# Kernel optimization log

Measured on AMD Instinct MI355X. Metric: run time of the kernel, lower is better.

## Reference

```python
import jax, jax.numpy as jnp
import numpy as np

B, S, D = 8, 2048, 512
MINF = 20000.0  # matches tf code's -20000.0 mask constant


def setup_inputs() -> dict:
    key = jax.random.key(0)
    k1, k2, k3 = jax.random.split(key, 3)
    x1 = jax.random.normal(k1, (B, S, D), dtype=jnp.float32)
    x2 = jax.random.normal(k2, (B, S, D), dtype=jnp.float32)
    # glorot_normal init for the learned (S, S) positional kernel
    std = np.sqrt(2.0 / (S + S)).astype(np.float32)
    kernel = jax.random.normal(k3, (S, S), dtype=jnp.float32) * std
    return {"x1": x1, "x2": x2, "kernel": kernel}


def reference(x1, x2, kernel):
    S_ = kernel.shape[0]
    # tf.matmul(kernel, inputs[i]) broadcasts (S,S) @ (B,S,D) -> (B,S,D)
    h1 = jnp.einsum('st,btd->bsd', kernel, x1)
    h2 = jnp.einsum('st,btd->bsd', kernel, x2)
    # att_scores: (B, S, S)
    scores = jnp.einsum('bsd,btd->bst', h1, h2)
    d_k = jnp.asarray(S_, dtype=scores.dtype) ** 0.5
    # upper_m[i,j] = -20000 for j > i (strictly upper), else 0; added BEFORE scaling
    row = jnp.arange(S_)
    mask = jnp.where(row[None, :] > row[:, None], -MINF, 0.0).astype(scores.dtype)
    attn = jax.nn.softmax((scores + mask) / d_k, axis=-1)
    # note: output attends over h1 (not h2), as in the original code
    return jnp.einsum('bst,btd->bsd', attn, h1)
```

## Files before the change

kernel.cpp:

```cpp
#include <hip/hip_runtime.h>
#include <hip/hip_bf16.h>

#define S_DIM 2048
#define D_DIM 512
#define B_DIM 8
#define SCALE 0.02209708691207961f

typedef __hip_bfloat16 bf16;
typedef short bf16x8 __attribute__((ext_vector_type(8)));
typedef float f32x4 __attribute__((ext_vector_type(4)));

__device__ __forceinline__ unsigned short f2b(float f) {
  __hip_bfloat16 h = __float2bfloat16(f);
  return __builtin_bit_cast(unsigned short, h);
}
__device__ __forceinline__ float b2f(unsigned short s) {
  return __bfloat162float(__builtin_bit_cast(__hip_bfloat16, s));
}

__device__ __forceinline__ void load_lds16(const void* g, void* l) {
  __builtin_amdgcn_global_load_lds((const __attribute__((address_space(1))) void*)g,
                                   (__attribute__((address_space(3))) void*)l, 16, 0, 0);
}

__global__ void prep(const float* __restrict__ x1, const float* __restrict__ x2,
                     const float* __restrict__ km,
                     bf16* __restrict__ xt, bf16* __restrict__ Kbf,
                     float* __restrict__ rowsum) {
  const int z = blockIdx.z;
  const int tid = threadIdx.x;
  if (z == 16) {
    const int bid = blockIdx.y * 8 + blockIdx.x;
    const float4* p = (const float4*)km;
    bf16x8* o = (bf16x8*)Kbf;
#pragma unroll
    for (int it = 0; it < 8; it++) {
      int i = bid * 2048 + it * 256 + tid;
      float4 a = p[2 * i], b = p[2 * i + 1];
      bf16x8 r;
      r[0] = f2b(a.x); r[1] = f2b(a.y); r[2] = f2b(a.z); r[3] = f2b(a.w);
      r[4] = f2b(b.x); r[5] = f2b(b.y); r[6] = f2b(b.z); r[7] = f2b(b.w);
      o[i] = r;
    }
    if (bid < 8) {
      float4 zf = {0.0f, 0.0f, 0.0f, 0.0f};
      float4* rp = (float4*)(rowsum + bid * 2048);
      rp[tid * 2] = zf;
      rp[tid * 2 + 1] = zf;
    }
    return;
  }
  __shared__ unsigned short t[64][66];
  const float* in = (z < 8 ? x1 : x2) + (size_t)(z & 7) * (S_DIM * D_DIM);
  bf16* ob = xt + (size_t)z * (size_t)(D_DIM * S_DIM);
  const int r0 = blockIdx.y * 64;
  const int c0 = blockIdx.x * 64;
  const int lr = tid >> 4, lq = tid & 15;
#pragma unroll
  for (int i = 0; i < 4; i++) {
    int r = i * 16 + lr;
    float4 v = *(const float4*)(in + (size_t)(r0 + r) * D_DIM + c0 + lq * 4);
    t[lq * 4 + 0][r] = f2b(v.x);
    t[lq * 4 + 1][r] = f2b(v.y);
    t[lq * 4 + 2][r] = f2b(v.z);
    t[lq * 4 + 3][r] = f2b(v.w);
  }
  __syncthreads();
#pragma unroll
  for (int j = 0; j < 4; j++) {
    int d = j * 16 + lr;
    const unsigned short* p = &t[d][lq * 4];
    uint2 u;
    u.x = (unsigned)p[0] | ((unsigned)p[1] << 16);
    u.y = (unsigned)p[2] | ((unsigned)p[3] << 16);
    *(uint2*)(ob + (size_t)(c0 + d) * S_DIM + r0 + lq * 4) = u;
  }
}

__global__ __launch_bounds__(512, 2) void gemm_h(
    const bf16* __restrict__ A, const bf16* __restrict__ X, bf16* __restrict__ H) {
  extern __shared__ char smem[];
  const int pid = blockIdx.x;
  const int mt = pid & 7;
  const int r_ = pid >> 3;
  const int ntile = r_ & 1;
  const int item = r_ >> 1;
  const int m0 = mt * 256, n0 = ntile * 256;
  const bf16* Xi = X + (size_t)item * (D_DIM * S_DIM);
  bf16* Hi = H + (size_t)item * (S_DIM * D_DIM);

  const int tid = threadIdx.x;
  const int w = tid >> 6, L = tid & 63;
  const int l15 = L & 15, lhi = L >> 4;
  const int wr = w >> 2, wn = w & 3;

  const int srow = tid >> 2;
  const int sslot = ((tid & 3) ^ ((tid >> 3) & 3)) * 8;
  const bf16* pA[2];
  const bf16* pB[2];
#pragma unroll
  for (int ld = 0; ld < 2; ld++) {
    pA[ld] = A + (size_t)(m0 + ld * 128 + srow) * 2048 + sslot;
    pB[ld] = Xi + (size_t)(n0 + ld * 128 + srow) * 2048 + sslot;
  }

  char* A0 = smem;          char* A1 = smem + 16384;  char* A2 = smem + 32768;
  char* B0 = smem + 49152;  char* B1 = smem + 65536;  char* B2 = smem + 81920;

  auto stage = [&](int t2, char* dA, char* dB) {
#pragma unroll
    for (int ld = 0; ld < 2; ld++)
      load_lds16(pA[ld] + t2 * 32, dA + ld * 8192 + w * 1024);
#pragma unroll
    for (int ld = 0; ld < 2; ld++)
      load_lds16(pB[ld] + t2 * 32, dB + ld * 8192 + w * 1024);
  };

  const int xo = (lhi ^ ((l15 >> 1) & 3)) << 4;
  int offA[8], offB[4];
#pragma unroll
  for (int m = 0; m < 8; m++) offA[m] = (wr * 128 + m * 16 + l15) * 64 + xo;
#pragma unroll
  for (int n = 0; n < 4; n++) offB[n] = (wn * 64 + n * 16 + l15) * 64 + xo;

  f32x4 acc[8][4];
#pragma unroll
  for (int m = 0; m < 8; m++)
#pragma unroll
    for (int n = 0; n < 4; n++) acc[m][n] = (f32x4){0, 0, 0, 0};

  stage(0, A0, B0);
  stage(1, A1, B1);

#pragma unroll 1
  for (int t = 0; t < 64; ++t) {
    if (t < 63) asm volatile("s_waitcnt vmcnt(4)" ::: "memory");
    else        asm volatile("s_waitcnt vmcnt(0)" ::: "memory");
    __builtin_amdgcn_s_barrier();
    asm volatile("" ::: "memory");
    if (t < 62) stage(t + 2, A2, B2);

    bf16x8 af[8], bfv[4];
#pragma unroll
    for (int m = 0; m < 8; m++) af[m] = *(const bf16x8*)(A0 + offA[m]);
#pragma unroll
    for (int n = 0; n < 4; n++) bfv[n] = *(const bf16x8*)(B0 + offB[n]);
    __builtin_amdgcn_s_setprio(1);
#pragma unroll
    for (int m = 0; m < 8; m++)
#pragma unroll
      for (int n = 0; n < 4; n++)
        acc[m][n] = __builtin_amdgcn_mfma_f32_16x16x32_bf16(bfv[n], af[m], acc[m][n], 0, 0, 0);
    __builtin_amdgcn_s_setprio(0);

    char* tA = A0; A0 = A1; A1 = A2; A2 = tA;
    char* tB = B0; B0 = B1; B1 = B2; B2 = tB;
  }

#pragma unroll
  for (int m = 0; m < 8; m++) {
    int grow = m0 + wr * 128 + m * 16 + l15;
#pragma unroll
    for (int n = 0; n < 4; n++) {
      int gcol = n0 + wn * 64 + n * 16 + lhi * 4;
      uint2 u;
      u.x = ((unsigned)f2b(acc[m][n][1]) << 16) | f2b(acc[m][n][0]);
      u.y = ((unsigned)f2b(acc[m][n][3]) << 16) | f2b(acc[m][n][2]);
      *(uint2*)(Hi + (size_t)grow * D_DIM + gcol) = u;
    }
  }
}

__global__ __launch_bounds__(512, 2) void gemm_score(
    const bf16* __restrict__ H1, const bf16* __restrict__ H2,
    bf16* __restrict__ E, float* __restrict__ rowsum, bf16* __restrict__ H1T) {
  extern __shared__ char smem[];
  const int pid = blockIdx.x;
  const int tid = threadIdx.x;

  if (pid >= 288) {
    const int tb = pid - 288;
    const int half = tid >> 8;
    const int t5 = tid & 255;
    unsigned short (*tl)[66] = (unsigned short (*)[66])(smem + half * 8448);
    const int lr = t5 >> 4, lq = t5 & 15;
#pragma unroll 1
    for (int i = 0; i < 4; i++) {
      const int tile = tb * 8 + half * 4 + i;
      const int z = tile >> 8;
      const int rem = tile & 255;
      const int r0 = (rem >> 3) * 64;
      const int c0 = (rem & 7) * 64;
      const bf16* ib = H1 + (size_t)z * (S_DIM * D_DIM);
      bf16* ob = H1T + (size_t)z * (S_DIM * D_DIM);
#pragma unroll
      for (int j = 0; j < 4; j++) {
        int r = j * 16 + lr;
        uint2 v = *(const uint2*)(ib + (size_t)(r0 + r) * D_DIM + c0 + lq * 4);
        tl[lq * 4 + 0][r] = (unsigned short)(v.x & 0xffff);
        tl[lq * 4 + 1][r] = (unsigned short)(v.x >> 16);
        tl[lq * 4 + 2][r] = (unsigned short)(v.y & 0xffff);
        tl[lq * 4 + 3][r] = (unsigned short)(v.y >> 16);
      }
      __syncthreads();
#pragma unroll
      for (int j = 0; j < 4; j++) {
        int d = j * 16 + lr;
        const unsigned short* p = &tl[d][lq * 4];
        uint2 u;
        u.x = (unsigned)p[0] | ((unsigned)p[1] << 16);
        u.y = (unsigned)p[2] | ((unsigned)p[3] << 16);
        *(uint2*)(ob + (size_t)(c0 + d) * S_DIM + r0 + lq * 4) = u;
      }
      __syncthreads();
    }
    return;
  }

  const int b = pid & 7;
  const int tri = pid >> 3;
  int mt = (int)((sqrtf(8.0f * (float)tri + 1.0f) - 1.0f) * 0.5f);
  while ((mt + 1) * (mt + 2) / 2 <= tri) mt++;
  while (mt * (mt + 1) / 2 > tri) mt--;
  const int nt = tri - mt * (mt + 1) / 2;
  const int m0 = mt * 256, n0 = nt * 256;
  const bool diag = (mt == nt);
  const bf16* Ab = H1 + (size_t)b * S_DIM * D_DIM;
  const bf16* Bb = H2 + (size_t)b * S_DIM * D_DIM;
  bf16* Eb = E + (size_t)b * S_DIM * S_DIM;
  float* rs = rowsum + b * S_DIM;

  const int w = tid >> 6, L = tid & 63;
  const int l15 = L & 15, lhi = L >> 4;
  const int wr = w >> 2, wn = w & 3;

  const int srow = tid >> 2;
  const int sslot = ((tid & 3) ^ ((tid >> 3) & 3)) * 8;
  const bf16* pA[2];
  const bf16* pB[2];
#pragma unroll
  for (int ld = 0; ld < 2; ld++) {
    pA[ld] = Ab + (size_t)(m0 + ld * 128 + srow) * D_DIM + sslot;
    pB[ld] = Bb + (size_t)(n0 + ld * 128 + srow) * D_DIM + sslot;
  }

  auto stage = [&](int t) {
    char* dA = smem + (t & 1) * 16384;
    char* dB = smem + 32768 + (t & 1) * 16384;
#pragma unroll
    for (int ld = 0; ld < 2; ld++)
      load_lds16(pA[ld] + t * 32, dA + ld * 8192 + w * 1024);
#pragma unroll
    for (int ld = 0; ld < 2; ld++)
      load_lds16(pB[ld] + t * 32, dB + ld * 8192 + w * 1024);
  };

  const int xo = (lhi ^ ((l15 >> 1) & 3)) << 4;
  int offA[8], offB[4];
#pragma unroll
  for (int m = 0; m < 8; m++) offA[m] = (wr * 128 + m * 16 + l15) * 64 + xo;
#pragma unroll
  for (int n = 0; n < 4; n++) offB[n] = (wn * 64 + n * 16 + l15) * 64 + xo;

  f32x4 acc[8][4];
#pragma unroll
  for (int m = 0; m < 8; m++)
#pragma unroll
    for (int n = 0; n < 4; n++) acc[m][n] = (f32x4){0, 0, 0, 0};

  stage(0);
#pragma unroll 2
  for (int t = 0; t < 16; ++t) {
    __syncthreads();
    if (t + 1 < 16) stage(t + 1);
    const char* bA = smem + (t & 1) * 16384;
    const char* bB = smem + 32768 + (t & 1) * 16384;
    bf16x8 af[8], bfv[4];
#pragma unroll
    for (int m = 0; m < 8; m++) af[m] = *(const bf16x8*)(bA + offA[m]);
#pragma unroll
    for (int n = 0; n < 4; n++) bfv[n] = *(const bf16x8*)(bB + offB[n]);
    __builtin_amdgcn_s_setprio(1);
#pragma unroll
    for (int m = 0; m < 8; m++)
#pragma unroll
      for (int n = 0; n < 4; n++)
        acc[m][n] = __builtin_amdgcn_mfma_f32_16x16x32_bf16(bfv[n], af[m], acc[m][n], 0, 0, 0);
    __builtin_amdgcn_s_setprio(0);
  }

#pragma unroll
  for (int m = 0; m < 8; m++) {
    int sg = m0 + wr * 128 + m * 16 + l15;
    float rp = 0.0f;
#pragma unroll
    for (int n = 0; n < 4; n++) {
      int tg0 = n0 + wn * 64 + n * 16 + lhi * 4;
      unsigned short e[4];
#pragma unroll
      for (int r = 0; r < 4; r++) {
        float v = (!diag || (tg0 + r) <= sg) ? __expf(acc[m][n][r] * SCALE) : 0.0f;
        e[r] = f2b(v);
        rp += b2f(e[r]);
      }
      uint2 u;
      u.x = ((unsigned)e[1] << 16) | e[0];
      u.y = ((unsigned)e[3] << 16) | e[2];
      *(uint2*)(Eb + (size_t)sg * S_DIM + tg0) = u;
    }
    rp += __shfl_xor(rp, 16);
    rp += __shfl_xor(rp, 32);
    if (lhi == 0) atomicAdd(rs + sg, rp);
  }
}

__global__ __launch_bounds__(256, 2) void gemm_pv(
    const bf16* __restrict__ E, const bf16* __restrict__ H1T,
    const float* __restrict__ rowsum, float* __restrict__ out) {
  extern __shared__ char smem[];
  const int pid = blockIdx.x;
  const int b = pid & 7;
  const int r_ = pid >> 3;
  const int nt = r_ & 3;
  const int mb = r_ >> 2;
  const int mt = (mb < 8) ? 2 * mb : 31 - 2 * mb;
  const int m0 = mt * 128, n0 = nt * 128;
  const int NT = (mt + 1) * 4;
  const bf16* Ab = E + (size_t)b * S_DIM * S_DIM + (size_t)m0 * S_DIM;
  const bf16* Bb = H1T + (size_t)b * D_DIM * S_DIM + (size_t)n0 * S_DIM;
  const float* rs = rowsum + b * S_DIM;
  float* Cb = out + (size_t)b * S_DIM * D_DIM;

  const int tid = threadIdx.x;
  const int w = tid >> 6, L = tid & 63;
  const int l15 = L & 15, lhi = L >> 4;
  const int wr = w >> 1, wc = w & 1;

  const int srow = tid >> 2;
  const int sslot = ((tid & 3) ^ ((tid >> 3) & 3)) * 8;
  const bf16* pA[2];
  const bf16* pB[2];
#pragma unroll
  for (int ld = 0; ld < 2; ld++) {
    pA[ld] = Ab + (size_t)(ld * 64 + srow) * S_DIM + sslot;
    pB[ld] = Bb + (size_t)(ld * 64 + srow) * S_DIM + sslot;
  }

  char* A0 = smem;          char* A1 = smem + 8192;   char* A2 = smem + 16384;
  char* B0 = smem + 24576;  char* B1 = smem + 32768;  char* B2 = smem + 40960;

  auto stage = [&](int t2, char* dA, char* dB) {
#pragma unroll
    for (int ld = 0; ld < 2; ld++)
      load_lds16(pA[ld] + t2 * 32, dA + ld * 4096 + w * 1024);
#pragma unroll
    for (int ld = 0; ld < 2; ld++)
      load_lds16(pB[ld] + t2 * 32, dB + ld * 4096 + w * 1024);
  };

  const int xo = (lhi ^ ((l15 >> 1) & 3)) << 4;
  int offA[4], offB[4];
#pragma unroll
  for (int m = 0; m < 4; m++) offA[m] = (wr * 64 + m * 16 + l15) * 64 + xo;
#pragma unroll
  for (int n = 0; n < 4; n++) offB[n] = (wc * 64 + n * 16 + l15) * 64 + xo;

  f32x4 acc[4][4];
#pragma unroll
  for (int m = 0; m < 4; m++)
#pragma unroll
    for (int n = 0; n < 4; n++) acc[m][n] = (f32x4){0, 0, 0, 0};

  stage(0, A0, B0);
  stage(1, A1, B1);

#pragma unroll 1
  for (int t = 0; t < NT; ++t) {
    if (t < NT - 1) asm volatile("s_waitcnt vmcnt(4)" ::: "memory");
    else            asm volatile("s_waitcnt vmcnt(0)" ::: "memory");
    __builtin_amdgcn_s_barrier();
    asm volatile("" ::: "memory");
    if (t + 2 < NT) stage(t + 2, A2, B2);

    bf16x8 af[4], bfv[4];
#pragma unroll
    for (int m = 0; m < 4; m++) af[m] = *(const bf16x8*)(A0 + offA[m]);
#pragma unroll
    for (int n = 0; n < 4; n++) bfv[n] = *(const bf16x8*)(B0 + offB[n]);
    __builtin_amdgcn_s_setprio(1);
#pragma unroll
    for (int m = 0; m < 4; m++)
#pragma unroll
      for (int n = 0; n < 4; n++)
        acc[m][n] = __builtin_amdgcn_mfma_f32_16x16x32_bf16(bfv[n], af[m], acc[m][n], 0, 0, 0);
    __builtin_amdgcn_s_setprio(0);

    char* tA = A0; A0 = A1; A1 = A2; A2 = tA;
    char* tB = B0; B0 = B1; B1 = B2; B2 = tB;
  }

#pragma unroll
  for (int m = 0; m < 4; m++) {
    int sg = m0 + wr * 64 + m * 16 + l15;
    float inv = 1.0f / rs[sg];
#pragma unroll
    for (int n = 0; n < 4; n++) {
      int gcol = n0 + wc * 64 + n * 16 + lhi * 4;
      float4 o;
      o.x = acc[m][n][0] * inv;
      o.y = acc[m][n][1] * inv;
      o.z = acc[m][n][2] * inv;
      o.w = acc[m][n][3] * inv;
      *(float4*)(Cb + (size_t)sg * D_DIM + gcol) = o;
    }
  }
}

extern "C" void kernel_launch(void* const* d_in, const int* in_sizes, int n_in,
                              void* d_out, int out_size, void* d_ws, size_t ws_size,
                              hipStream_t stream) {
  const float* x1 = (const float*)d_in[0];
  const float* x2 = (const float*)d_in[1];
  const float* km = (const float*)d_in[2];
  float* out = (float*)d_out;
  char* ws = (char*)d_ws;
  bf16* E    = (bf16*)(ws);
  bf16* Kbf  = (bf16*)(ws);
  bf16* x1t  = (bf16*)(ws + (8ull << 20));
  bf16* h1n  = (bf16*)(ws + (64ull << 20));
  bf16* h2n  = (bf16*)(ws + (80ull << 20));
  bf16* h1t  = (bf16*)(ws + (96ull << 20));
  float* rowsum = (float*)(ws + (112ull << 20));

  prep<<<dim3(8, 32, 17), 256, 0, stream>>>(x1, x2, km, x1t, Kbf, rowsum);
  gemm_h<<<256, 512, 98304, stream>>>(Kbf, x1t, h1n);
  gemm_score<<<544, 512, 65536, stream>>>(h1n, h2n, E, rowsum, h1t);
  gemm_pv<<<512, 256, 49152, stream>>>(E, h1t, rowsum, out);
}
```

Measured before the change: 166.0 us.

## Double-buffer gemm_h with K=64 stages instead of triple-buffered K=32

Restructures the gemm_h K-loop from a three-deep ring of 32-wide K stages to two buffers of 64-wide K stages. This halves the number of barriers and loop iterations, and each stage runs two MFMA sub-steps with an XOR swizzle matched to the 128-byte rows. Shared memory grows to 128KB and the launch bound drops to one block per CU. The risk is lost occupancy and less latency hiding, since each iteration now waits on vmcnt(0) right before its barrier.

```diff
diff --git a/kernel.cpp b/kernel.cpp
--- a/kernel.cpp
+++ b/kernel.cpp
@@ -77,7 +77,7 @@
   }
 }
 
-__global__ __launch_bounds__(512, 2) void gemm_h(
+__global__ __launch_bounds__(512, 1) void gemm_h(
     const bf16* __restrict__ A, const bf16* __restrict__ X, bf16* __restrict__ H) {
   extern __shared__ char smem[];
   const int pid = blockIdx.x;
@@ -94,34 +94,35 @@
   const int l15 = L & 15, lhi = L >> 4;
   const int wr = w >> 2, wn = w & 3;
 
-  const int srow = tid >> 2;
-  const int sslot = ((tid & 3) ^ ((tid >> 3) & 3)) * 8;
-  const bf16* pA[2];
-  const bf16* pB[2];
-#pragma unroll
-  for (int ld = 0; ld < 2; ld++) {
-    pA[ld] = A + (size_t)(m0 + ld * 128 + srow) * 2048 + sslot;
-    pB[ld] = Xi + (size_t)(n0 + ld * 128 + srow) * 2048 + sslot;
-  }
-
-  char* A0 = smem;          char* A1 = smem + 16384;  char* A2 = smem + 32768;
-  char* B0 = smem + 49152;  char* B1 = smem + 65536;  char* B2 = smem + 81920;
-
-  auto stage = [&](int t2, char* dA, char* dB) {
-#pragma unroll
-    for (int ld = 0; ld < 2; ld++)
-      load_lds16(pA[ld] + t2 * 32, dA + ld * 8192 + w * 1024);
-#pragma unroll
-    for (int ld = 0; ld < 2; ld++)
-      load_lds16(pB[ld] + t2 * 32, dB + ld * 8192 + w * 1024);
+  const int srow = tid >> 3;
+  const int sslot = ((tid & 7) ^ (srow & 7)) * 8;
+  const bf16* pA[4];
+  const bf16* pB[4];
+#pragma unroll
+  for (int ld = 0; ld < 4; ld++) {
+    pA[ld] = A + (size_t)(m0 + ld * 64 + srow) * 2048 + sslot;
+    pB[ld] = Xi + (size_t)(n0 + ld * 64 + srow) * 2048 + sslot;
+  }
+
+  auto stage = [&](int t) {
+    char* dA = smem + (t & 1) * 32768 + w * 1024;
+    char* dB = smem + 65536 + (t & 1) * 32768 + w * 1024;
+    const int ko = t * 64;
+#pragma unroll
+    for (int ld = 0; ld < 4; ld++) {
+      load_lds16(pA[ld] + ko, dA + ld * 8192);
+      load_lds16(pB[ld] + ko, dB + ld * 8192);
+    }
   };
 
-  const int xo = (lhi ^ ((l15 >> 1) & 3)) << 4;
-  int offA[8], offB[4];
-#pragma unroll
-  for (int m = 0; m < 8; m++) offA[m] = (wr * 128 + m * 16 + l15) * 64 + xo;
-#pragma unroll
-  for (int n = 0; n < 4; n++) offB[n] = (wn * 64 + n * 16 + l15) * 64 + xo;
+  const int xsw = l15 & 7;
+  int offA0[8], offB0[4];
+#pragma unroll
+  for (int m = 0; m < 8; m++)
+    offA0[m] = (wr * 128 + m * 16 + l15) * 128 + ((lhi ^ xsw) << 4);
+#pragma unroll
+  for (int n = 0; n < 4; n++)
+    offB0[n] = (wn * 64 + n * 16 + l15) * 128 + ((lhi ^ xsw) << 4);
 
   f32x4 acc[8][4];
 #pragma unroll
@@ -129,32 +130,34 @@
 #pragma unroll
     for (int n = 0; n < 4; n++) acc[m][n] = (f32x4){0, 0, 0, 0};
 
-  stage(0, A0, B0);
-  stage(1, A1, B1);
+  stage(0);
+  asm volatile("s_waitcnt vmcnt(0)" ::: "memory");
+  __builtin_amdgcn_s_barrier();
+  asm volatile("" ::: "memory");
 
 #pragma unroll 1
-  for (int t = 0; t < 64; ++t) {
-    if (t < 63) asm volatile("s_waitcnt vmcnt(4)" ::: "memory");
-    else        asm volatile("s_waitcnt vmcnt(0)" ::: "memory");
+  for (int t = 0; t < 32; ++t) {
+    if (t + 1 < 32) stage(t + 1);
+    const char* bA = smem + (t & 1) * 32768;
+    const char* bB = smem + 65536 + (t & 1) * 32768;
+#pragma unroll
+    for (int kk = 0; kk < 2; kk++) {
+      bf16x8 af[8], bfv[4];
+#pragma unroll
+      for (int m = 0; m < 8; m++) af[m] = *(const bf16x8*)(bA + (offA0[m] ^ (kk << 6)));
+#pragma unroll
+      for (int n = 0; n < 4; n++) bfv[n] = *(const bf16x8*)(bB + (offB0[n] ^ (kk << 6)));
+      __builtin_amdgcn_s_setprio(1);
+#pragma unroll
+      for (int m = 0; m < 8; m++)
+#pragma unroll
+        for (int n = 0; n < 4; n++)
+          acc[m][n] = __builtin_amdgcn_mfma_f32_16x16x32_bf16(bfv[n], af[m], acc[m][n], 0, 0, 0);
+      __builtin_amdgcn_s_setprio(0);
+    }
+    asm volatile("s_waitcnt vmcnt(0)" ::: "memory");
     __builtin_amdgcn_s_barrier();
     asm volatile("" ::: "memory");
-    if (t < 62) stage(t + 2, A2, B2);
-
-    bf16x8 af[8], bfv[4];
-#pragma unroll
-    for (int m = 0; m < 8; m++) af[m] = *(const bf16x8*)(A0 + offA[m]);
-#pragma unroll
-    for (int n = 0; n < 4; n++) bfv[n] = *(const bf16x8*)(B0 + offB[n]);
-    __builtin_amdgcn_s_setprio(1);
-#pragma unroll
-    for (int m = 0; m < 8; m++)
-#pragma unroll
-      for (int n = 0; n < 4; n++)
-        acc[m][n] = __builtin_amdgcn_mfma_f32_16x16x32_bf16(bfv[n], af[m], acc[m][n], 0, 0, 0);
-    __builtin_amdgcn_s_setprio(0);
-
-    char* tA = A0; A0 = A1; A1 = A2; A2 = tA;
-    char* tB = B0; B0 = B1; B1 = B2; B2 = tB;
   }
 
 #pragma unroll
@@ -433,7 +436,7 @@
   float* rowsum = (float*)(ws + (112ull << 20));
 
   prep<<<dim3(8, 32, 17), 256, 0, stream>>>(x1, x2, km, x1t, Kbf, rowsum);
-  gemm_h<<<256, 512, 98304, stream>>>(Kbf, x1t, h1n);
+  gemm_h<<<256, 512, 131072, stream>>>(Kbf, x1t, h1n);
   gemm_score<<<544, 512, 65536, stream>>>(h1n, h2n, E, rowsum, h1t);
   gemm_pv<<<512, 256, 49152, stream>>>(E, h1t, rowsum, out);
 }
```

Result: no change. 163.3 us (-1.7%).
